# Kernel optimization log

Measured on AMD Instinct MI355X. Metric: run time of the kernel, lower is better.

## Reference

```python
import jax, jax.numpy as jnp
import numpy as np

N_BUCKET, EPB, EMBED, K, TAU = 64, 8, 1024, 2, 1.0
EPS_NORM, EPS_W = 1e-12, 1e-9

def _l2norm(x):
    n = jnp.linalg.norm(x, axis=-1, keepdims=True)
    return x / jnp.maximum(n, EPS_NORM)

def setup_inputs() -> dict:
    key = jax.random.key(0)
    k1, k2, k3 = jax.random.split(key, 3)
    h = jax.random.normal(k1, (8, 2048, EMBED), dtype=jnp.float32)
    op_id = jax.random.randint(k2, (8, 2048), 0, N_BUCKET, dtype=jnp.int64)
    expert_key = jax.random.normal(k3, (N_BUCKET, EPB, EMBED), dtype=jnp.float32) / np.sqrt(EMBED)
    return {"h": h, "op_id": op_id, "expert_key": expert_key}

def reference(h, op_id, expert_key):
    # h: (B,T,C), op_id: (B,T), expert_key: (n_bucket, epb, C)
    bucket = jnp.clip(op_id, 0, N_BUCKET - 1)          # (B,T)
    h_n = _l2norm(h)                                    # (B,T,C)
    keys = _l2norm(expert_key)                          # (nb,epb,C)
    keys_bt = keys[bucket]                              # gather -> (B,T,epb,C)
    score = jnp.einsum('btc,btec->bte', h_n, keys_bt)   # (B,T,epb)
    score = score / max(TAU, 1e-6)
    probs_local = jax.nn.softmax(score, axis=-1)        # (B,T,epb)
    topv, local = jax.lax.top_k(probs_local, K)         # (B,T,k) each
    w = topv / (jnp.sum(topv, axis=-1, keepdims=True) + EPS_W)
    gid = bucket[..., None] * EPB + local               # (B,T,k) global expert ids
    return (gid, w)
```

## Files before the change

### kernel.cpp

```cpp
#include <hip/hip_runtime.h>
#include <cmath>

#define EMBED   1024
#define EPB     8
#define NB      64
#define KTOP    2

__global__ void key_rnorm_kernel(const float* __restrict__ ek,
                                 float* __restrict__ rnorm) {
    int wave = (int)((blockIdx.x * blockDim.x + threadIdx.x) >> 6);
    int lane = threadIdx.x & 63;
    if (wave >= NB * EPB) return;
    const float4* row = (const float4*)(ek + (size_t)wave * EMBED);
    float s = 0.f;
#pragma unroll
    for (int c = 0; c < 4; ++c) {
        float4 v = row[c * 64 + lane];
        s += v.x * v.x + v.y * v.y + v.z * v.z + v.w * v.w;
    }
#pragma unroll
    for (int off = 32; off; off >>= 1) s += __shfl_xor(s, off, 64);
    if (lane == 0) rnorm[wave] = 1.0f / fmaxf(sqrtf(s), 1e-12f);
}

__global__ __launch_bounds__(256, 6) void router_duo_kernel(
    const float* __restrict__ h, const int* __restrict__ op,
    const float* __restrict__ ek, const float* __restrict__ rk,
    float* __restrict__ out_gid, float* __restrict__ out_w, int ntok) {
    int gtid = blockIdx.x * blockDim.x + threadIdx.x;
    int wid  = gtid >> 6;
    int lane = threadIdx.x & 63;
    int half = lane >> 5;
    int r    = lane & 31;
    int tq   = wid * 2 + half;
    int tc   = min(tq, ntok - 1);

    int b = op[tc];
    b = min(max(b, 0), NB - 1);

    const float4* hrow = (const float4*)(h + (size_t)tc * EMBED);
    const float4* kb   = (const float4*)ek + (size_t)b * (EPB * EMBED / 4);

    float dot[EPB] = {0.f, 0.f, 0.f, 0.f, 0.f, 0.f, 0.f, 0.f};
    float hh = 0.f;
#pragma unroll
    for (int i = 0; i < 8; ++i) {
        float4 a = hrow[i * 32 + r];
        hh += a.x * a.x + a.y * a.y + a.z * a.z + a.w * a.w;
#pragma unroll
        for (int e = 0; e < EPB; ++e) {
            float4 kv = kb[e * 256 + i * 32 + r];
            dot[e] += a.x * kv.x + a.y * kv.y + a.z * kv.z + a.w * kv.w;
        }
    }

#pragma unroll
    for (int off = 16; off; off >>= 1) {
        hh += __shfl_xor(hh, off, 64);
#pragma unroll
        for (int e = 0; e < EPB; ++e) dot[e] += __shfl_xor(dot[e], off, 64);
    }

    float rh = 1.0f / fmaxf(sqrtf(hh), 1e-12f);
    float sc[EPB];
    float m = -1e30f;
#pragma unroll
    for (int e = 0; e < EPB; ++e) {
        sc[e] = dot[e] * rh * rk[b * EPB + e];
        m = fmaxf(m, sc[e]);
    }
    float ex[EPB];
    float Z = 0.f;
#pragma unroll
    for (int e = 0; e < EPB; ++e) { ex[e] = expf(sc[e] - m); Z += ex[e]; }

    int i1 = 0;
#pragma unroll
    for (int e = 1; e < EPB; ++e) if (ex[e] > ex[i1]) i1 = e;
    int i2 = (i1 == 0) ? 1 : 0;
#pragma unroll
    for (int e = 0; e < EPB; ++e)
        if (e != i1 && ex[e] > ex[i2]) i2 = e;

    if (r == 0 && tq < ntok) {
        float p1 = ex[i1] / Z;
        float p2 = ex[i2] / Z;
        float ws = p1 + p2 + 1e-9f;
        ((float2*)out_gid)[tq] =
            make_float2((float)(b * EPB + i1), (float)(b * EPB + i2));
        ((float2*)out_w)[tq] = make_float2(p1 / ws, p2 / ws);
    }
}

extern "C" void kernel_launch(void* const* d_in, const int* in_sizes, int n_in,
                              void* d_out, int out_size, void* d_ws, size_t ws_size,
                              hipStream_t stream) {
    const float* h     = (const float*)d_in[0];
    const int*   op_id = (const int*)  d_in[1];
    const float* ek    = (const float*)d_in[2];

    int ntok = in_sizes[1];

    float* rk      = (float*)d_ws;
    float* out_gid = (float*)d_out;
    float* out_w   = out_gid + (size_t)ntok * KTOP;

    key_rnorm_kernel<<<128, 256, 0, stream>>>(ek, rk);

    int blocks = (ntok + 7) / 8;
    router_duo_kernel<<<blocks, 256, 0, stream>>>(h, op_id, ek, rk,
                                                  out_gid, out_w, ntok);
}
```

Measured before the change: 126.0 us.

## Bucket-sort tokens and keep each bucket's expert keys in registers

Adds a single-block binning kernel that histograms op_id, prefix-sums per-bucket counts and builds a token permutation grouped by bucket, split into 8-token chunks. A new router kernel gives each wave one chunk: it loads that bucket's 8 expert keys into registers once, computes the key norms inline, then loops over the 8 tokens. Previously every token re-read its 32 KB of keys from cache. This is meant to cut that repeated key traffic and drop the separate key-norm kernel. In exchange it adds a serial single-block binning pass, scattered output writes, and low occupancy from heavy register use. The old path remains as a fallback when the workspace is too small.

```diff
diff --git a/kernel.cpp b/kernel.cpp
--- a/kernel.cpp
+++ b/kernel.cpp
@@ -5,6 +5,157 @@
 #define EPB     8
 #define NB      64
 #define KTOP    2
+#define TPW     8
+
+__global__ __launch_bounds__(1024) void bin_kernel(
+    const int* __restrict__ op, int ntok,
+    int* __restrict__ bstart_g, int* __restrict__ cnt_g,
+    int* __restrict__ cpre_g, int* __restrict__ chunk2b,
+    int* __restrict__ perm) {
+    __shared__ int s_hist[NB];
+    __shared__ int s_cur[NB];
+    int tid = threadIdx.x, lane = tid & 63;
+    if (tid < NB) s_hist[tid] = 0;
+    __syncthreads();
+    for (int i = tid; i < ntok; i += 1024) {
+        int b = min(max(op[i], 0), NB - 1);
+        atomicAdd(&s_hist[b], 1);
+    }
+    __syncthreads();
+    if (tid < 64) {
+        int c   = s_hist[tid];
+        int nch = (c + TPW - 1) / TPW;
+        int ic = c, in = nch;
+#pragma unroll
+        for (int off = 1; off < 64; off <<= 1) {
+            int vc = __shfl_up(ic, off, 64);
+            int vn = __shfl_up(in, off, 64);
+            if (lane >= off) { ic += vc; in += vn; }
+        }
+        int bs = ic - c;
+        int cp = in - nch;
+        s_cur[tid]    = bs;
+        bstart_g[tid] = bs;
+        cnt_g[tid]    = c;
+        cpre_g[tid]   = cp;
+        if (tid == 63) cpre_g[NB] = in;
+        for (int j = 0; j < nch; ++j) chunk2b[cp + j] = tid;
+    }
+    __syncthreads();
+    for (int i = tid; i < ntok; i += 1024) {
+        int b = min(max(op[i], 0), NB - 1);
+        int pos = atomicAdd(&s_cur[b], 1);
+        perm[pos] = i;
+    }
+}
+
+__global__ __launch_bounds__(256, 2) void router_regkey_kernel(
+    const float* __restrict__ h, const float* __restrict__ ek,
+    const int* __restrict__ perm, const int* __restrict__ bstart_g,
+    const int* __restrict__ cnt_g, const int* __restrict__ cpre_g,
+    const int* __restrict__ chunk2b,
+    float* __restrict__ out_gid, float* __restrict__ out_w) {
+    int gtid = blockIdx.x * blockDim.x + threadIdx.x;
+    int wid  = gtid >> 6;
+    int lane = threadIdx.x & 63;
+    int total = cpre_g[NB];
+    if (wid >= total) return;
+
+    int b    = chunk2b[wid];
+    int lc   = wid - cpre_g[b];
+    int base = bstart_g[b] + lc * TPW;
+    int end  = bstart_g[b] + cnt_g[b];
+
+    const float4* kb = (const float4*)ek + (size_t)b * (EPB * EMBED / 4);
+    float4 kv[EPB * 4];
+#pragma unroll
+    for (int e = 0; e < EPB; ++e)
+#pragma unroll
+        for (int i = 0; i < 4; ++i)
+            kv[e * 4 + i] = kb[e * 256 + i * 64 + lane];
+
+    float rke[EPB];
+#pragma unroll
+    for (int e = 0; e < EPB; ++e) {
+        float s = 0.f;
+#pragma unroll
+        for (int i = 0; i < 4; ++i) {
+            float4 v = kv[e * 4 + i];
+            s += v.x * v.x + v.y * v.y + v.z * v.z + v.w * v.w;
+        }
+        rke[e] = s;
+    }
+#pragma unroll
+    for (int off = 32; off; off >>= 1)
+#pragma unroll
+        for (int e = 0; e < EPB; ++e) rke[e] += __shfl_xor(rke[e], off, 64);
+#pragma unroll
+    for (int e = 0; e < EPB; ++e)
+        rke[e] = 1.0f / fmaxf(sqrtf(rke[e]), 1e-12f);
+
+    int tok[TPW];
+#pragma unroll
+    for (int t = 0; t < TPW; ++t) tok[t] = perm[min(base + t, end - 1)];
+
+#pragma unroll
+    for (int t = 0; t < TPW; ++t) {
+        const float4* hrow = (const float4*)(h + (size_t)tok[t] * EMBED);
+        float4 hv[4];
+#pragma unroll
+        for (int c = 0; c < 4; ++c) hv[c] = hrow[c * 64 + lane];
+
+        float hh = 0.f;
+        float dot[EPB] = {0.f, 0.f, 0.f, 0.f, 0.f, 0.f, 0.f, 0.f};
+#pragma unroll
+        for (int c = 0; c < 4; ++c) {
+            float4 a = hv[c];
+            hh += a.x * a.x + a.y * a.y + a.z * a.z + a.w * a.w;
+#pragma unroll
+            for (int e = 0; e < EPB; ++e) {
+                float4 k4 = kv[e * 4 + c];
+                dot[e] += a.x * k4.x + a.y * k4.y + a.z * k4.z + a.w * k4.w;
+            }
+        }
+
+#pragma unroll
+        for (int off = 32; off; off >>= 1) {
+            hh += __shfl_xor(hh, off, 64);
+#pragma unroll
+            for (int e = 0; e < EPB; ++e) dot[e] += __shfl_xor(dot[e], off, 64);
+        }
+
+        float rh = 1.0f / fmaxf(sqrtf(hh), 1e-12f);
+        float sc[EPB];
+        float m = -1e30f;
+#pragma unroll
+        for (int e = 0; e < EPB; ++e) {
+            sc[e] = dot[e] * rh * rke[e];
+            m = fmaxf(m, sc[e]);
+        }
+        float ex[EPB];
+        float Z = 0.f;
+#pragma unroll
+        for (int e = 0; e < EPB; ++e) { ex[e] = expf(sc[e] - m); Z += ex[e]; }
+
+        int i1 = 0;
+#pragma unroll
+        for (int e = 1; e < EPB; ++e) if (ex[e] > ex[i1]) i1 = e;
+        int i2 = (i1 == 0) ? 1 : 0;
+#pragma unroll
+        for (int e = 0; e < EPB; ++e)
+            if (e != i1 && ex[e] > ex[i2]) i2 = e;
+
+        if (lane == 0 && (base + t) < end) {
+            float p1 = ex[i1] / Z;
+            float p2 = ex[i2] / Z;
+            float ws = p1 + p2 + 1e-9f;
+            int tk = tok[t];
+            ((float2*)out_gid)[tk] =
+                make_float2((float)(b * EPB + i1), (float)(b * EPB + i2));
+            ((float2*)out_w)[tk] = make_float2(p1 / ws, p2 / ws);
+        }
+    }
+}
 
 __global__ void key_rnorm_kernel(const float* __restrict__ ek,
                                  float* __restrict__ rnorm) {
@@ -49,18 +200,16 @@
         hh += a.x * a.x + a.y * a.y + a.z * a.z + a.w * a.w;
 #pragma unroll
         for (int e = 0; e < EPB; ++e) {
-            float4 kv = kb[e * 256 + i * 32 + r];
-            dot[e] += a.x * kv.x + a.y * kv.y + a.z * kv.z + a.w * kv.w;
-        }
-    }
-
+            float4 kvv = kb[e * 256 + i * 32 + r];
+            dot[e] += a.x * kvv.x + a.y * kvv.y + a.z * kvv.z + a.w * kvv.w;
+        }
+    }
 #pragma unroll
     for (int off = 16; off; off >>= 1) {
         hh += __shfl_xor(hh, off, 64);
 #pragma unroll
         for (int e = 0; e < EPB; ++e) dot[e] += __shfl_xor(dot[e], off, 64);
     }
-
     float rh = 1.0f / fmaxf(sqrtf(hh), 1e-12f);
     float sc[EPB];
     float m = -1e30f;
@@ -73,7 +222,6 @@
     float Z = 0.f;
 #pragma unroll
     for (int e = 0; e < EPB; ++e) { ex[e] = expf(sc[e] - m); Z += ex[e]; }
-
     int i1 = 0;
 #pragma unroll
     for (int e = 1; e < EPB; ++e) if (ex[e] > ex[i1]) i1 = e;
@@ -81,7 +229,6 @@
 #pragma unroll
     for (int e = 0; e < EPB; ++e)
         if (e != i1 && ex[e] > ex[i2]) i2 = e;
-
     if (r == 0 && tq < ntok) {
         float p1 = ex[i1] / Z;
         float p2 = ex[i2] / Z;
@@ -99,15 +246,31 @@
     const int*   op_id = (const int*)  d_in[1];
     const float* ek    = (const float*)d_in[2];
 
-    int ntok = in_sizes[1];
-
-    float* rk      = (float*)d_ws;
+    int ntok  = in_sizes[1];
+    int maxch = NB + (ntok + TPW - 1) / TPW;
+
     float* out_gid = (float*)d_out;
     float* out_w   = out_gid + (size_t)ntok * KTOP;
 
-    key_rnorm_kernel<<<128, 256, 0, stream>>>(ek, rk);
-
-    int blocks = (ntok + 7) / 8;
-    router_duo_kernel<<<blocks, 256, 0, stream>>>(h, op_id, ek, rk,
-                                                  out_gid, out_w, ntok);
-}
+    float* rk      = (float*)d_ws;
+    int*   bstart  = (int*)(rk + 512);
+    int*   cnt     = bstart + NB;
+    int*   cpre    = cnt + NB;
+    int*   chunk2b = cpre + (NB + 1);
+    int*   perm    = chunk2b + maxch;
+    size_t need    = ((size_t)(512 + 2 * NB + NB + 1 + maxch) + (size_t)ntok) * 4;
+
+    if (ws_size < need) {
+        key_rnorm_kernel<<<128, 256, 0, stream>>>(ek, rk);
+        int blocks2 = (ntok + 7) / 8;
+        router_duo_kernel<<<blocks2, 256, 0, stream>>>(h, op_id, ek, rk,
+                                                       out_gid, out_w, ntok);
+        return;
+    }
+
+    bin_kernel<<<1, 1024, 0, stream>>>(op_id, ntok, bstart, cnt, cpre,
+                                       chunk2b, perm);
+    int blocks = (maxch * 64 + 255) / 256;
+    router_regkey_kernel<<<blocks, 256, 0, stream>>>(
+        h, ek, perm, bstart, cnt, cpre, chunk2b, out_gid, out_w);
+}
```

Result: slower. 156.9 us (+24.5%).

## Group tokens by bucket and stage expert keys in shared memory per chunk

Applied to the files above, without the earlier changes.

Adds a counting-sort pipeline (histogram, scan, scatter) that groups tokens by bucket into a permutation, then routes chunks of 16 same-bucket tokens per block. Each block loads its bucket's 8x1024 key slice into LDS once and has each wave compute 4 tokens against it, so key reuse moves from L2/L1 into shared memory. The cost is four extra small launches, global atomics, and gathered h rows. The old path remains as a fallback when workspace is too small.

```diff
diff --git a/kernel.cpp b/kernel.cpp
--- a/kernel.cpp
+++ b/kernel.cpp
@@ -1,10 +1,211 @@
 #include <hip/hip_runtime.h>
 #include <cmath>
 
-#define EMBED   1024
-#define EPB     8
-#define NB      64
-#define KTOP    2
+#define EMBED 1024
+#define EPB   8
+#define NB    64
+#define KTOP  2
+#define CHT   16
+#define HB    16
+
+__global__ void zero_kernel(int* __restrict__ count) {
+    if (threadIdx.x < NB) count[threadIdx.x] = 0;
+}
+
+__global__ __launch_bounds__(256) void prep1_kernel(
+    const float* __restrict__ ek, float* __restrict__ rnorm,
+    const int* __restrict__ op, int ntok, int* __restrict__ count) {
+    int tid = threadIdx.x;
+    if (blockIdx.x < 128) {
+        int row  = blockIdx.x * 4 + (tid >> 6);
+        int lane = tid & 63;
+        const float4* r4 = (const float4*)(ek + (size_t)row * EMBED);
+        float s = 0.f;
+#pragma unroll
+        for (int c = 0; c < 4; ++c) {
+            float4 v = r4[c * 64 + lane];
+            s += v.x * v.x + v.y * v.y + v.z * v.z + v.w * v.w;
+        }
+#pragma unroll
+        for (int off = 32; off; off >>= 1) s += __shfl_xor(s, off, 64);
+        if (lane == 0) rnorm[row] = 1.0f / fmaxf(sqrtf(s), 1e-12f);
+        return;
+    }
+    __shared__ int hc[NB];
+    int hb = blockIdx.x - 128;
+    if (tid < NB) hc[tid] = 0;
+    __syncthreads();
+    for (int i = hb * 256 + tid; i < ntok; i += HB * 256) {
+        int b = min(max(op[i], 0), NB - 1);
+        atomicAdd(&hc[b], 1);
+    }
+    __syncthreads();
+    if (tid < NB && hc[tid]) atomicAdd(&count[tid], hc[tid]);
+}
+
+__global__ void scan_kernel(const int* __restrict__ count,
+                            int* __restrict__ bstart, int* __restrict__ soffs,
+                            int* __restrict__ cpre, int* __restrict__ chunk2b) {
+    int tid = threadIdx.x;
+    int c   = count[tid];
+    int nch = (c + CHT - 1) / CHT;
+    int ic = c, in = nch;
+#pragma unroll
+    for (int off = 1; off < 64; off <<= 1) {
+        int vc = __shfl_up(ic, off, 64);
+        int vn = __shfl_up(in, off, 64);
+        if (tid >= off) { ic += vc; in += vn; }
+    }
+    int bs = ic - c, cp = in - nch;
+    bstart[tid] = bs; soffs[tid] = bs; cpre[tid] = cp;
+    if (tid == 63) cpre[NB] = in;
+    for (int j = 0; j < nch; ++j) chunk2b[cp + j] = tid;
+}
+
+__global__ void scatter_kernel(const int* __restrict__ op, int ntok,
+                               int* __restrict__ soffs, int* __restrict__ perm) {
+    for (int i = blockIdx.x * blockDim.x + threadIdx.x; i < ntok;
+         i += gridDim.x * blockDim.x) {
+        int b = min(max(op[i], 0), NB - 1);
+        int pos = atomicAdd(&soffs[b], 1);
+        perm[pos] = i;
+    }
+}
+
+#define D4(a,b) ((a).x*(b).x + (a).y*(b).y + (a).z*(b).z + (a).w*(b).w)
+
+#define ITER(i) { \
+    int off = (i)*64 + lane; \
+    float4 a0 = hr0[off]; float4 a1 = hr1[off]; \
+    float4 a2 = hr2[off]; float4 a3 = hr3[off]; \
+    float4 q0 = skv[0*256+off]; float4 q1 = skv[1*256+off]; \
+    float4 q2 = skv[2*256+off]; float4 q3 = skv[3*256+off]; \
+    float4 q4 = skv[4*256+off]; float4 q5 = skv[5*256+off]; \
+    float4 q6 = skv[6*256+off]; float4 q7 = skv[7*256+off]; \
+    hh0 += D4(a0,a0); hh1 += D4(a1,a1); hh2 += D4(a2,a2); hh3 += D4(a3,a3); \
+    d00 += D4(a0,q0); d01 += D4(a0,q1); d02 += D4(a0,q2); d03 += D4(a0,q3); \
+    d04 += D4(a0,q4); d05 += D4(a0,q5); d06 += D4(a0,q6); d07 += D4(a0,q7); \
+    d10 += D4(a1,q0); d11 += D4(a1,q1); d12 += D4(a1,q2); d13 += D4(a1,q3); \
+    d14 += D4(a1,q4); d15 += D4(a1,q5); d16 += D4(a1,q6); d17 += D4(a1,q7); \
+    d20 += D4(a2,q0); d21 += D4(a2,q1); d22 += D4(a2,q2); d23 += D4(a2,q3); \
+    d24 += D4(a2,q4); d25 += D4(a2,q5); d26 += D4(a2,q6); d27 += D4(a2,q7); \
+    d30 += D4(a3,q0); d31 += D4(a3,q1); d32 += D4(a3,q2); d33 += D4(a3,q3); \
+    d34 += D4(a3,q4); d35 += D4(a3,q5); d36 += D4(a3,q6); d37 += D4(a3,q7); }
+
+#define RED(o) \
+    hh0 += __shfl_xor(hh0,o,64); hh1 += __shfl_xor(hh1,o,64); \
+    hh2 += __shfl_xor(hh2,o,64); hh3 += __shfl_xor(hh3,o,64); \
+    d00 += __shfl_xor(d00,o,64); d01 += __shfl_xor(d01,o,64); \
+    d02 += __shfl_xor(d02,o,64); d03 += __shfl_xor(d03,o,64); \
+    d04 += __shfl_xor(d04,o,64); d05 += __shfl_xor(d05,o,64); \
+    d06 += __shfl_xor(d06,o,64); d07 += __shfl_xor(d07,o,64); \
+    d10 += __shfl_xor(d10,o,64); d11 += __shfl_xor(d11,o,64); \
+    d12 += __shfl_xor(d12,o,64); d13 += __shfl_xor(d13,o,64); \
+    d14 += __shfl_xor(d14,o,64); d15 += __shfl_xor(d15,o,64); \
+    d16 += __shfl_xor(d16,o,64); d17 += __shfl_xor(d17,o,64); \
+    d20 += __shfl_xor(d20,o,64); d21 += __shfl_xor(d21,o,64); \
+    d22 += __shfl_xor(d22,o,64); d23 += __shfl_xor(d23,o,64); \
+    d24 += __shfl_xor(d24,o,64); d25 += __shfl_xor(d25,o,64); \
+    d26 += __shfl_xor(d26,o,64); d27 += __shfl_xor(d27,o,64); \
+    d30 += __shfl_xor(d30,o,64); d31 += __shfl_xor(d31,o,64); \
+    d32 += __shfl_xor(d32,o,64); d33 += __shfl_xor(d33,o,64); \
+    d34 += __shfl_xor(d34,o,64); d35 += __shfl_xor(d35,o,64); \
+    d36 += __shfl_xor(d36,o,64); d37 += __shfl_xor(d37,o,64);
+
+#define SEL4(x0,x1,x2,x3) ((g==0)?(x0):(g==1)?(x1):(g==2)?(x2):(x3))
+#define T1(e) if (ex##e > v1) { v1 = ex##e; i1 = (e); }
+#define T2(e) if ((e) != i1 && ex##e > v2) { v2 = ex##e; i2 = (e); }
+
+__global__ __launch_bounds__(256, 4) void router_chunk_kernel(
+    const float* __restrict__ h, const float* __restrict__ ek,
+    const float* __restrict__ rk, const int* __restrict__ perm,
+    const int* __restrict__ bstart_g, const int* __restrict__ cnt_g,
+    const int* __restrict__ cpre_g, const int* __restrict__ chunk2b,
+    float* __restrict__ out_gid, float* __restrict__ out_w) {
+    __shared__ float sk[EPB * EMBED];
+    int tid  = threadIdx.x;
+    int lane = tid & 63;
+    int wave = tid >> 6;
+    int g    = lane >> 4;
+    int r16  = lane & 15;
+
+    int gch = blockIdx.x;
+    if (gch >= cpre_g[NB]) return;
+    int b    = chunk2b[gch];
+    int lc   = gch - cpre_g[b];
+    int base = bstart_g[b] + lc * CHT;
+    int end  = bstart_g[b] + cnt_g[b];
+
+    const float4* src = (const float4*)ek + (size_t)b * (EPB * EMBED / 4);
+    float4* dst = (float4*)sk;
+#pragma unroll
+    for (int j = 0; j < 8; ++j) dst[j * 256 + tid] = src[j * 256 + tid];
+
+    float rk0 = rk[b*EPB+0], rk1 = rk[b*EPB+1], rk2 = rk[b*EPB+2], rk3 = rk[b*EPB+3];
+    float rk4 = rk[b*EPB+4], rk5 = rk[b*EPB+5], rk6 = rk[b*EPB+6], rk7 = rk[b*EPB+7];
+    int s0i = base + wave * 4;
+    int tok0 = perm[min(s0i + 0, end - 1)];
+    int tok1 = perm[min(s0i + 1, end - 1)];
+    int tok2 = perm[min(s0i + 2, end - 1)];
+    int tok3 = perm[min(s0i + 3, end - 1)];
+    const float4* hr0 = (const float4*)(h + (size_t)tok0 * EMBED);
+    const float4* hr1 = (const float4*)(h + (size_t)tok1 * EMBED);
+    const float4* hr2 = (const float4*)(h + (size_t)tok2 * EMBED);
+    const float4* hr3 = (const float4*)(h + (size_t)tok3 * EMBED);
+    __syncthreads();
+
+    const float4* skv = (const float4*)sk;
+    float hh0=0.f, hh1=0.f, hh2=0.f, hh3=0.f;
+    float d00=0.f,d01=0.f,d02=0.f,d03=0.f,d04=0.f,d05=0.f,d06=0.f,d07=0.f;
+    float d10=0.f,d11=0.f,d12=0.f,d13=0.f,d14=0.f,d15=0.f,d16=0.f,d17=0.f;
+    float d20=0.f,d21=0.f,d22=0.f,d23=0.f,d24=0.f,d25=0.f,d26=0.f,d27=0.f;
+    float d30=0.f,d31=0.f,d32=0.f,d33=0.f,d34=0.f,d35=0.f,d36=0.f,d37=0.f;
+
+    ITER(0) ITER(1) ITER(2) ITER(3)
+
+    RED(32) RED(16) RED(8) RED(4) RED(2) RED(1)
+
+    float thh = SEL4(hh0, hh1, hh2, hh3);
+    float t0 = SEL4(d00, d10, d20, d30);
+    float t1 = SEL4(d01, d11, d21, d31);
+    float t2 = SEL4(d02, d12, d22, d32);
+    float t3 = SEL4(d03, d13, d23, d33);
+    float t4 = SEL4(d04, d14, d24, d34);
+    float t5 = SEL4(d05, d15, d25, d35);
+    float t6 = SEL4(d06, d16, d26, d36);
+    float t7 = SEL4(d07, d17, d27, d37);
+    int   tk = SEL4(tok0, tok1, tok2, tok3);
+    int   gi = s0i + g;
+
+    float rh = 1.0f / fmaxf(sqrtf(thh), 1e-12f);
+    float sc0 = t0 * rh * rk0, sc1 = t1 * rh * rk1;
+    float sc2 = t2 * rh * rk2, sc3 = t3 * rh * rk3;
+    float sc4 = t4 * rh * rk4, sc5 = t5 * rh * rk5;
+    float sc6 = t6 * rh * rk6, sc7 = t7 * rh * rk7;
+    float m = -1e30f;
+    m = fmaxf(m, sc0); m = fmaxf(m, sc1); m = fmaxf(m, sc2); m = fmaxf(m, sc3);
+    m = fmaxf(m, sc4); m = fmaxf(m, sc5); m = fmaxf(m, sc6); m = fmaxf(m, sc7);
+    float ex0 = expf(sc0 - m), ex1 = expf(sc1 - m);
+    float ex2 = expf(sc2 - m), ex3 = expf(sc3 - m);
+    float ex4 = expf(sc4 - m), ex5 = expf(sc5 - m);
+    float ex6 = expf(sc6 - m), ex7 = expf(sc7 - m);
+    float Z = 0.f;
+    Z += ex0; Z += ex1; Z += ex2; Z += ex3;
+    Z += ex4; Z += ex5; Z += ex6; Z += ex7;
+    float v1 = ex0; int i1 = 0;
+    T1(1) T1(2) T1(3) T1(4) T1(5) T1(6) T1(7)
+    float v2 = (i1 == 0) ? ex1 : ex0;
+    int   i2 = (i1 == 0) ? 1 : 0;
+    T2(0) T2(1) T2(2) T2(3) T2(4) T2(5) T2(6) T2(7)
+
+    if (r16 == 0 && gi < end) {
+        float p1 = v1 / Z, p2 = v2 / Z;
+        float ws = p1 + p2 + 1e-9f;
+        ((float2*)out_gid)[tk] =
+            make_float2((float)(b * EPB + i1), (float)(b * EPB + i2));
+        ((float2*)out_w)[tk] = make_float2(p1 / ws, p2 / ws);
+    }
+}
 
 __global__ void key_rnorm_kernel(const float* __restrict__ ek,
                                  float* __restrict__ rnorm) {
@@ -34,33 +235,28 @@
     int r    = lane & 31;
     int tq   = wid * 2 + half;
     int tc   = min(tq, ntok - 1);
-
     int b = op[tc];
     b = min(max(b, 0), NB - 1);
-
     const float4* hrow = (const float4*)(h + (size_t)tc * EMBED);
     const float4* kb   = (const float4*)ek + (size_t)b * (EPB * EMBED / 4);
-
-    float dot[EPB] = {0.f, 0.f, 0.f, 0.f, 0.f, 0.f, 0.f, 0.f};
+    float dot[EPB] = {0.f,0.f,0.f,0.f,0.f,0.f,0.f,0.f};
     float hh = 0.f;
 #pragma unroll
     for (int i = 0; i < 8; ++i) {
         float4 a = hrow[i * 32 + r];
-        hh += a.x * a.x + a.y * a.y + a.z * a.z + a.w * a.w;
+        hh += a.x*a.x + a.y*a.y + a.z*a.z + a.w*a.w;
 #pragma unroll
         for (int e = 0; e < EPB; ++e) {
             float4 kv = kb[e * 256 + i * 32 + r];
-            dot[e] += a.x * kv.x + a.y * kv.y + a.z * kv.z + a.w * kv.w;
+            dot[e] += a.x*kv.x + a.y*kv.y + a.z*kv.z + a.w*kv.w;
         }
     }
-
 #pragma unroll
     for (int off = 16; off; off >>= 1) {
         hh += __shfl_xor(hh, off, 64);
 #pragma unroll
         for (int e = 0; e < EPB; ++e) dot[e] += __shfl_xor(dot[e], off, 64);
     }
-
     float rh = 1.0f / fmaxf(sqrtf(hh), 1e-12f);
     float sc[EPB];
     float m = -1e30f;
@@ -73,7 +269,6 @@
     float Z = 0.f;
 #pragma unroll
     for (int e = 0; e < EPB; ++e) { ex[e] = expf(sc[e] - m); Z += ex[e]; }
-
     int i1 = 0;
 #pragma unroll
     for (int e = 1; e < EPB; ++e) if (ex[e] > ex[i1]) i1 = e;
@@ -81,10 +276,8 @@
 #pragma unroll
     for (int e = 0; e < EPB; ++e)
         if (e != i1 && ex[e] > ex[i2]) i2 = e;
-
     if (r == 0 && tq < ntok) {
-        float p1 = ex[i1] / Z;
-        float p2 = ex[i2] / Z;
+        float p1 = ex[i1] / Z, p2 = ex[i2] / Z;
         float ws = p1 + p2 + 1e-9f;
         ((float2*)out_gid)[tq] =
             make_float2((float)(b * EPB + i1), (float)(b * EPB + i2));
@@ -99,15 +292,33 @@
     const int*   op_id = (const int*)  d_in[1];
     const float* ek    = (const float*)d_in[2];
 
-    int ntok = in_sizes[1];
-
-    float* rk      = (float*)d_ws;
+    int ntok  = in_sizes[1];
+    int maxch = NB + (ntok + CHT - 1) / CHT;
+
     float* out_gid = (float*)d_out;
     float* out_w   = out_gid + (size_t)ntok * KTOP;
 
-    key_rnorm_kernel<<<128, 256, 0, stream>>>(ek, rk);
-
-    int blocks = (ntok + 7) / 8;
-    router_duo_kernel<<<blocks, 256, 0, stream>>>(h, op_id, ek, rk,
-                                                  out_gid, out_w, ntok);
-}
+    float* rk      = (float*)d_ws;
+    int*   count   = (int*)(rk + 512);
+    int*   bstart  = count  + NB;
+    int*   soffs   = bstart + NB;
+    int*   cpre    = soffs  + NB;
+    int*   chunk2b = cpre + (NB + 1);
+    int*   perm    = chunk2b + maxch;
+    size_t need    = ((size_t)(512 + 3 * NB + NB + 1 + maxch) + (size_t)ntok) * 4;
+
+    if (ws_size < need) {
+        key_rnorm_kernel<<<128, 256, 0, stream>>>(ek, rk);
+        int blocks2 = (ntok + 7) / 8;
+        router_duo_kernel<<<blocks2, 256, 0, stream>>>(h, op_id, ek, rk,
+                                                       out_gid, out_w, ntok);
+        return;
+    }
+
+    zero_kernel<<<1, 64, 0, stream>>>(count);
+    prep1_kernel<<<128 + HB, 256, 0, stream>>>(ek, rk, op_id, ntok, count);
+    scan_kernel<<<1, 64, 0, stream>>>(count, bstart, soffs, cpre, chunk2b);
+    scatter_kernel<<<HB, 256, 0, stream>>>(op_id, ntok, soffs, perm);
+    router_chunk_kernel<<<maxch, 256, 0, stream>>>(
+        h, ek, rk, perm, bstart, count, cpre, chunk2b, out_gid, out_w);
+}
```

New measurement: 143.6 us. 14.0% more time.

## Bucket tokens per block and stage expert keys in shared memory

Applied to the files above, without the earlier changes.

Replaces the two-kernel design with a single kernel where each block owns one bucket and a slice of tokens. The block loads that bucket's 8 expert keys into LDS, computes their norms in-block, compacts the matching token indices with a shared atomic counter, and then has each wave process 4 tokens at a time against the shared keys. This removes the separate norm launch and the per-token global gathers of key rows. In exchange, every block scans the op_id slice, and each wave holds 36 accumulators in registers, which limits occupancy.

```diff
diff --git a/kernel.cpp b/kernel.cpp
--- a/kernel.cpp
+++ b/kernel.cpp
@@ -1,94 +1,171 @@
 #include <hip/hip_runtime.h>
 #include <cmath>
 
-#define EMBED   1024
-#define EPB     8
-#define NB      64
-#define KTOP    2
+#define EMBED 1024
+#define EPB   8
+#define NB    64
+#define KTOP  2
+#define SLICE 1024
 
-__global__ void key_rnorm_kernel(const float* __restrict__ ek,
-                                 float* __restrict__ rnorm) {
-    int wave = (int)((blockIdx.x * blockDim.x + threadIdx.x) >> 6);
-    int lane = threadIdx.x & 63;
-    if (wave >= NB * EPB) return;
-    const float4* row = (const float4*)(ek + (size_t)wave * EMBED);
-    float s = 0.f;
+#define D4(a,b) ((a).x*(b).x + (a).y*(b).y + (a).z*(b).z + (a).w*(b).w)
+
+#define ITER(i) { \
+    int off = (i)*64 + lane; \
+    float4 a0 = hr0[off]; float4 a1 = hr1[off]; \
+    float4 a2 = hr2[off]; float4 a3 = hr3[off]; \
+    float4 q0 = skv[0*256+off]; float4 q1 = skv[1*256+off]; \
+    float4 q2 = skv[2*256+off]; float4 q3 = skv[3*256+off]; \
+    float4 q4 = skv[4*256+off]; float4 q5 = skv[5*256+off]; \
+    float4 q6 = skv[6*256+off]; float4 q7 = skv[7*256+off]; \
+    hh0 += D4(a0,a0); hh1 += D4(a1,a1); hh2 += D4(a2,a2); hh3 += D4(a3,a3); \
+    d00 += D4(a0,q0); d01 += D4(a0,q1); d02 += D4(a0,q2); d03 += D4(a0,q3); \
+    d04 += D4(a0,q4); d05 += D4(a0,q5); d06 += D4(a0,q6); d07 += D4(a0,q7); \
+    d10 += D4(a1,q0); d11 += D4(a1,q1); d12 += D4(a1,q2); d13 += D4(a1,q3); \
+    d14 += D4(a1,q4); d15 += D4(a1,q5); d16 += D4(a1,q6); d17 += D4(a1,q7); \
+    d20 += D4(a2,q0); d21 += D4(a2,q1); d22 += D4(a2,q2); d23 += D4(a2,q3); \
+    d24 += D4(a2,q4); d25 += D4(a2,q5); d26 += D4(a2,q6); d27 += D4(a2,q7); \
+    d30 += D4(a3,q0); d31 += D4(a3,q1); d32 += D4(a3,q2); d33 += D4(a3,q3); \
+    d34 += D4(a3,q4); d35 += D4(a3,q5); d36 += D4(a3,q6); d37 += D4(a3,q7); }
+
+#define RED(o) \
+    hh0 += __shfl_xor(hh0,o,64); hh1 += __shfl_xor(hh1,o,64); \
+    hh2 += __shfl_xor(hh2,o,64); hh3 += __shfl_xor(hh3,o,64); \
+    d00 += __shfl_xor(d00,o,64); d01 += __shfl_xor(d01,o,64); \
+    d02 += __shfl_xor(d02,o,64); d03 += __shfl_xor(d03,o,64); \
+    d04 += __shfl_xor(d04,o,64); d05 += __shfl_xor(d05,o,64); \
+    d06 += __shfl_xor(d06,o,64); d07 += __shfl_xor(d07,o,64); \
+    d10 += __shfl_xor(d10,o,64); d11 += __shfl_xor(d11,o,64); \
+    d12 += __shfl_xor(d12,o,64); d13 += __shfl_xor(d13,o,64); \
+    d14 += __shfl_xor(d14,o,64); d15 += __shfl_xor(d15,o,64); \
+    d16 += __shfl_xor(d16,o,64); d17 += __shfl_xor(d17,o,64); \
+    d20 += __shfl_xor(d20,o,64); d21 += __shfl_xor(d21,o,64); \
+    d22 += __shfl_xor(d22,o,64); d23 += __shfl_xor(d23,o,64); \
+    d24 += __shfl_xor(d24,o,64); d25 += __shfl_xor(d25,o,64); \
+    d26 += __shfl_xor(d26,o,64); d27 += __shfl_xor(d27,o,64); \
+    d30 += __shfl_xor(d30,o,64); d31 += __shfl_xor(d31,o,64); \
+    d32 += __shfl_xor(d32,o,64); d33 += __shfl_xor(d33,o,64); \
+    d34 += __shfl_xor(d34,o,64); d35 += __shfl_xor(d35,o,64); \
+    d36 += __shfl_xor(d36,o,64); d37 += __shfl_xor(d37,o,64);
+
+#define SEL4(x0,x1,x2,x3) ((g==0)?(x0):(g==1)?(x1):(g==2)?(x2):(x3))
+#define T1(e) if (ex##e > v1) { v1 = ex##e; i1 = (e); }
+#define T2(e) if ((e) != i1 && ex##e > v2) { v2 = ex##e; i2 = (e); }
+
+__global__ __launch_bounds__(256, 4) void router_mono_kernel(
+    const float* __restrict__ h, const int* __restrict__ op,
+    const float* __restrict__ ek,
+    float* __restrict__ out_gid, float* __restrict__ out_w,
+    int ntok, int nslice) {
+    __shared__ float sk[EPB * EMBED];
+    __shared__ float s_rk[EPB];
+    __shared__ int   s_list[SLICE];
+    __shared__ int   s_cnt;
+
+    int tid  = threadIdx.x;
+    int lane = tid & 63;
+    int wave = tid >> 6;
+    int g    = lane >> 4;
+    int r16  = lane & 15;
+
+    int b  = blockIdx.x / nslice;
+    int sl = blockIdx.x - b * nslice;
+
+    const float4* src = (const float4*)ek + (size_t)b * (EPB * EMBED / 4);
+    float4* dst = (float4*)sk;
 #pragma unroll
-    for (int c = 0; c < 4; ++c) {
-        float4 v = row[c * 64 + lane];
-        s += v.x * v.x + v.y * v.y + v.z * v.z + v.w * v.w;
-    }
-#pragma unroll
-    for (int off = 32; off; off >>= 1) s += __shfl_xor(s, off, 64);
-    if (lane == 0) rnorm[wave] = 1.0f / fmaxf(sqrtf(s), 1e-12f);
-}
-
-__global__ __launch_bounds__(256, 6) void router_duo_kernel(
-    const float* __restrict__ h, const int* __restrict__ op,
-    const float* __restrict__ ek, const float* __restrict__ rk,
-    float* __restrict__ out_gid, float* __restrict__ out_w, int ntok) {
-    int gtid = blockIdx.x * blockDim.x + threadIdx.x;
-    int wid  = gtid >> 6;
-    int lane = threadIdx.x & 63;
-    int half = lane >> 5;
-    int r    = lane & 31;
-    int tq   = wid * 2 + half;
-    int tc   = min(tq, ntok - 1);
-
-    int b = op[tc];
-    b = min(max(b, 0), NB - 1);
-
-    const float4* hrow = (const float4*)(h + (size_t)tc * EMBED);
-    const float4* kb   = (const float4*)ek + (size_t)b * (EPB * EMBED / 4);
-
-    float dot[EPB] = {0.f, 0.f, 0.f, 0.f, 0.f, 0.f, 0.f, 0.f};
-    float hh = 0.f;
-#pragma unroll
-    for (int i = 0; i < 8; ++i) {
-        float4 a = hrow[i * 32 + r];
-        hh += a.x * a.x + a.y * a.y + a.z * a.z + a.w * a.w;
-#pragma unroll
-        for (int e = 0; e < EPB; ++e) {
-            float4 kv = kb[e * 256 + i * 32 + r];
-            dot[e] += a.x * kv.x + a.y * kv.y + a.z * kv.z + a.w * kv.w;
-        }
-    }
+    for (int j = 0; j < 8; ++j) dst[j * 256 + tid] = src[j * 256 + tid];
+    if (tid == 0) s_cnt = 0;
 
 #pragma unroll
-    for (int off = 16; off; off >>= 1) {
-        hh += __shfl_xor(hh, off, 64);
+    for (int rr = 0; rr < 2; ++rr) {
+        int row = wave * 2 + rr;
+        const float4* r4 = (const float4*)(ek + (size_t)(b * EPB + row) * EMBED);
+        float s = 0.f;
 #pragma unroll
-        for (int e = 0; e < EPB; ++e) dot[e] += __shfl_xor(dot[e], off, 64);
+        for (int c = 0; c < 4; ++c) {
+            float4 v = r4[c * 64 + lane];
+            s += v.x * v.x + v.y * v.y + v.z * v.z + v.w * v.w;
+        }
+#pragma unroll
+        for (int off = 32; off; off >>= 1) s += __shfl_xor(s, off, 64);
+        if (lane == 0) s_rk[row] = 1.0f / fmaxf(sqrtf(s), 1e-12f);
     }
+    __syncthreads();
 
-    float rh = 1.0f / fmaxf(sqrtf(hh), 1e-12f);
-    float sc[EPB];
-    float m = -1e30f;
-#pragma unroll
-    for (int e = 0; e < EPB; ++e) {
-        sc[e] = dot[e] * rh * rk[b * EPB + e];
-        m = fmaxf(m, sc[e]);
+    int t0 = sl * SLICE;
+    int t1 = min(t0 + SLICE, ntok);
+    for (int i = t0 + tid; i < t1; i += 256) {
+        int ob = min(max(op[i], 0), NB - 1);
+        if (ob == b) { int p = atomicAdd(&s_cnt, 1); s_list[p] = i; }
     }
-    float ex[EPB];
-    float Z = 0.f;
-#pragma unroll
-    for (int e = 0; e < EPB; ++e) { ex[e] = expf(sc[e] - m); Z += ex[e]; }
+    __syncthreads();
+    int cnt = s_cnt;
 
-    int i1 = 0;
-#pragma unroll
-    for (int e = 1; e < EPB; ++e) if (ex[e] > ex[i1]) i1 = e;
-    int i2 = (i1 == 0) ? 1 : 0;
-#pragma unroll
-    for (int e = 0; e < EPB; ++e)
-        if (e != i1 && ex[e] > ex[i2]) i2 = e;
+    float rk0 = s_rk[0], rk1 = s_rk[1], rk2 = s_rk[2], rk3 = s_rk[3];
+    float rk4 = s_rk[4], rk5 = s_rk[5], rk6 = s_rk[6], rk7 = s_rk[7];
+    const float4* skv = (const float4*)sk;
 
-    if (r == 0 && tq < ntok) {
-        float p1 = ex[i1] / Z;
-        float p2 = ex[i2] / Z;
-        float ws = p1 + p2 + 1e-9f;
-        ((float2*)out_gid)[tq] =
-            make_float2((float)(b * EPB + i1), (float)(b * EPB + i2));
-        ((float2*)out_w)[tq] = make_float2(p1 / ws, p2 / ws);
+    for (int base = 0; base < cnt; base += 16) {
+        int i0   = base + wave * 4;
+        int tok0 = s_list[min(i0 + 0, cnt - 1)];
+        int tok1 = s_list[min(i0 + 1, cnt - 1)];
+        int tok2 = s_list[min(i0 + 2, cnt - 1)];
+        int tok3 = s_list[min(i0 + 3, cnt - 1)];
+        const float4* hr0 = (const float4*)(h + (size_t)tok0 * EMBED);
+        const float4* hr1 = (const float4*)(h + (size_t)tok1 * EMBED);
+        const float4* hr2 = (const float4*)(h + (size_t)tok2 * EMBED);
+        const float4* hr3 = (const float4*)(h + (size_t)tok3 * EMBED);
+
+        float hh0=0.f, hh1=0.f, hh2=0.f, hh3=0.f;
+        float d00=0.f,d01=0.f,d02=0.f,d03=0.f,d04=0.f,d05=0.f,d06=0.f,d07=0.f;
+        float d10=0.f,d11=0.f,d12=0.f,d13=0.f,d14=0.f,d15=0.f,d16=0.f,d17=0.f;
+        float d20=0.f,d21=0.f,d22=0.f,d23=0.f,d24=0.f,d25=0.f,d26=0.f,d27=0.f;
+        float d30=0.f,d31=0.f,d32=0.f,d33=0.f,d34=0.f,d35=0.f,d36=0.f,d37=0.f;
+
+        ITER(0) ITER(1) ITER(2) ITER(3)
+
+        RED(32) RED(16) RED(8) RED(4) RED(2) RED(1)
+
+        float thh = SEL4(hh0, hh1, hh2, hh3);
+        float t0s = SEL4(d00, d10, d20, d30);
+        float t1s = SEL4(d01, d11, d21, d31);
+        float t2s = SEL4(d02, d12, d22, d32);
+        float t3s = SEL4(d03, d13, d23, d33);
+        float t4s = SEL4(d04, d14, d24, d34);
+        float t5s = SEL4(d05, d15, d25, d35);
+        float t6s = SEL4(d06, d16, d26, d36);
+        float t7s = SEL4(d07, d17, d27, d37);
+        int   tk  = SEL4(tok0, tok1, tok2, tok3);
+        int   gi  = i0 + g;
+
+        float rh = 1.0f / fmaxf(sqrtf(thh), 1e-12f);
+        float sc0 = t0s * rh * rk0, sc1 = t1s * rh * rk1;
+        float sc2 = t2s * rh * rk2, sc3 = t3s * rh * rk3;
+        float sc4 = t4s * rh * rk4, sc5 = t5s * rh * rk5;
+        float sc6 = t6s * rh * rk6, sc7 = t7s * rh * rk7;
+        float m = -1e30f;
+        m = fmaxf(m, sc0); m = fmaxf(m, sc1); m = fmaxf(m, sc2); m = fmaxf(m, sc3);
+        m = fmaxf(m, sc4); m = fmaxf(m, sc5); m = fmaxf(m, sc6); m = fmaxf(m, sc7);
+        float ex0 = expf(sc0 - m), ex1 = expf(sc1 - m);
+        float ex2 = expf(sc2 - m), ex3 = expf(sc3 - m);
+        float ex4 = expf(sc4 - m), ex5 = expf(sc5 - m);
+        float ex6 = expf(sc6 - m), ex7 = expf(sc7 - m);
+        float Z = 0.f;
+        Z += ex0; Z += ex1; Z += ex2; Z += ex3;
+        Z += ex4; Z += ex5; Z += ex6; Z += ex7;
+        float v1 = ex0; int i1 = 0;
+        T1(1) T1(2) T1(3) T1(4) T1(5) T1(6) T1(7)
+        float v2 = (i1 == 0) ? ex1 : ex0;
+        int   i2 = (i1 == 0) ? 1 : 0;
+        T2(0) T2(1) T2(2) T2(3) T2(4) T2(5) T2(6) T2(7)
+
+        if (r16 == 0 && gi < cnt) {
+            float p1 = v1 / Z, p2 = v2 / Z;
+            float ws = p1 + p2 + 1e-9f;
+            ((float2*)out_gid)[tk] =
+                make_float2((float)(b * EPB + i1), (float)(b * EPB + i2));
+            ((float2*)out_w)[tk] = make_float2(p1 / ws, p2 / ws);
+        }
     }
 }
 
@@ -101,13 +178,10 @@
 
     int ntok = in_sizes[1];
 
-    float* rk      = (float*)d_ws;
     float* out_gid = (float*)d_out;
     float* out_w   = out_gid + (size_t)ntok * KTOP;
 
-    key_rnorm_kernel<<<128, 256, 0, stream>>>(ek, rk);
-
-    int blocks = (ntok + 7) / 8;
-    router_duo_kernel<<<blocks, 256, 0, stream>>>(h, op_id, ek, rk,
-                                                  out_gid, out_w, ntok);
+    int nslice = (ntok + SLICE - 1) / SLICE;
+    router_mono_kernel<<<NB * nslice, 256, 0, stream>>>(
+        h, op_id, ek, out_gid, out_w, ntok, nslice);
 }
```

After: 196.3 us. 55.8% more time.
